# Performance work log

Measured on AMD Instinct MI355X. Metric: run time of the kernel, lower is better.

The kernel has to match this reference:

```python
import jax, jax.numpy as jnp
import numpy as np

N = 100000
E = 1600000
IN_F = 128
OUT_F = 32
HEADS = 6
NEG_SLOPE = 0.2


def setup_inputs() -> dict:
    key = jax.random.key(0)
    k1, k2, k3, k4, k5 = jax.random.split(key, 5)
    x = jax.random.normal(k1, (N, IN_F), dtype=jnp.float32)
    edge_index = jax.random.randint(k2, (2, E), 0, N, dtype=jnp.int64)
    # GATConv params (PyG layout): shared linear for src/dst, per-head attention vectors, bias
    glorot = lambda k, shape: jax.random.normal(k, shape, dtype=jnp.float32) * np.sqrt(2.0 / (shape[0] + shape[-1]))
    W = glorot(k3, (IN_F, HEADS * OUT_F))          # lin.weight^T
    att_src = glorot(k4, (HEADS, OUT_F)) * 0.1     # [H, C]
    att_dst = glorot(k5, (HEADS, OUT_F)) * 0.1
    bias = jnp.zeros((OUT_F,), dtype=jnp.float32)  # concat=False -> bias of size out_feature
    return {"x": x, "edge_index": edge_index, "W": W,
            "att_src": att_src, "att_dst": att_dst, "bias": bias}


def reference(x, edge_index, W, att_src, att_dst, bias):
    src, dst = edge_index[0], edge_index[1]
    # Linear projection to per-head features: [N, H, C]
    xp = (x @ W).reshape(N, HEADS, OUT_F)
    # Per-node attention logit halves: [N, H]
    a_s = jnp.einsum("nhc,hc->nh", xp, att_src)
    a_d = jnp.einsum("nhc,hc->nh", xp, att_dst)
    # Per-edge logits with LeakyReLU: [E, H]
    e = jax.nn.leaky_relu(a_s[src] + a_d[dst], negative_slope=NEG_SLOPE)
    # Segment softmax over edges grouped by destination node
    m = jax.ops.segment_max(e, dst, num_segments=N)            # [N, H]
    m = jnp.where(jnp.isfinite(m), m, 0.0)                     # empty segments -> -inf guard
    e = jnp.exp(e - m[dst])
    s = jax.ops.segment_sum(e, dst, num_segments=N)            # [N, H]
    alpha = e / (s[dst] + 1e-16)                               # [E, H]
    # Weighted scatter-add aggregation: [N, H, C]
    msg = xp[src] * alpha[:, :, None]
    out = jax.ops.segment_sum(msg, dst, num_segments=N)
    # concat=False -> mean over heads, add bias, then SELU
    out = out.mean(axis=1) + bias
    return jax.nn.selu(out)
```

## Files before the change

### kernel.cpp

```cpp
#include <hip/hip_runtime.h>


typedef __attribute__((ext_vector_type(8))) short short8;
typedef __attribute__((ext_vector_type(4))) float f32x4;

#define SK 136
#define SLOTS 48

__device__ __forceinline__ unsigned short f2bf(float f)
{
    unsigned int u = __float_as_uint(f);
    u = (u + 0x7fffu + ((u >> 16) & 1u)) >> 16;
    return (unsigned short)u;
}

__global__ __launch_bounds__(256) void k_prep(
    const float* __restrict__ W,
    const float* __restrict__ att_src, const float* __restrict__ att_dst,
    unsigned short* __restrict__ wat, unsigned short* __restrict__ Wb,
    int* __restrict__ deg, int N)
{
    int i = blockIdx.x * 256 + threadIdx.x;
    if (i < N) deg[i] = 0;
    if (i < 128 * 192) Wb[i] = f2bf(W[i]);
    if (i < 128 * 16) {
        int k = i >> 4, c = i & 15;
        float v = 0.f;
        if (c < 12) {
            int h = c < 6 ? c : c - 6;
            const float* av = (c < 6 ? att_src : att_dst) + h * 32;
            const float* wr = W + k * 192 + h * 32;
            #pragma unroll
            for (int j = 0; j < 32; ++j) v = fmaf(wr[j], av[j], v);
        }
        wat[i] = f2bf(v);
    }
}

__global__ __launch_bounds__(256) void k_gd(
    const float* __restrict__ x, const unsigned short* __restrict__ Wb,
    const unsigned short* __restrict__ wat,
    char* __restrict__ xpb, float* __restrict__ sc,
    float* __restrict__ a_s, float* __restrict__ a_d,
    const int* __restrict__ ei, int* __restrict__ deg, int* __restrict__ csr,
    int N, int E, int GB, int DB)
{
    __shared__ __align__(16) unsigned short xt[64 * SK];
    __shared__ unsigned int smax[64 * 6];
    const int t   = threadIdx.x;
    const int bid = (int)blockIdx.x >> 1;

    if (blockIdx.x & 1) {
        if (bid >= DB) return;
        const int G = DB * 256;
        const int gid = bid * 256 + t;
        int s[4], d[4], r[4];
        #pragma unroll
        for (int k = 0; k < 4; ++k) {
            int e = gid + k * G;
            bool ok = e < E;
            int ec = ok ? e : 0;
            s[k] = ei[ec];
            d[k] = ei[E + ec];
            if (!ok) d[k] = -1;
        }
        #pragma unroll
        for (int k = 0; k < 4; ++k)
            r[k] = (d[k] >= 0) ? atomicAdd(&deg[d[k]], 1) : SLOTS;
        #pragma unroll
        for (int k = 0; k < 4; ++k)
            if (r[k] < SLOTS && d[k] >= 0) csr[d[k] * SLOTS + r[k]] = s[k];
        return;
    }

    if (bid >= GB) return;
    const int wave = t >> 6;
    const int lane = t & 63;
    const int ln   = lane & 15;
    const int q    = lane >> 4;
    const int n0   = bid * 64;
    const int cb   = wave * 48;

    {
        const float4* x4 = (const float4*)x;
        #pragma unroll
        for (int it = 0; it < 8; ++it) {
            int i   = t + it * 256;
            int row = i >> 5;
            int c4  = i & 31;
            int gr  = n0 + row;
            if (gr > N - 1) gr = N - 1;
            float4 f = x4[(size_t)gr * 32 + c4];
            unsigned int u0 = (unsigned int)f2bf(f.x) | ((unsigned int)f2bf(f.y) << 16);
            unsigned int u1 = (unsigned int)f2bf(f.z) | ((unsigned int)f2bf(f.w) << 16);
            *(uint2*)(xt + row * SK + c4 * 4) = make_uint2(u0, u1);
        }
        if (t < 128) { smax[t] = 0u; smax[t + 128] = 0u; smax[t + 256] = 0u; }
    }

    short8 bw[3][4];
    #pragma unroll
    for (int nt = 0; nt < 3; ++nt)
        #pragma unroll
        for (int kbi = 0; kbi < 4; ++kbi) {
            short8 v;
            #pragma unroll
            for (int j = 0; j < 8; ++j)
                v[j] = (short)Wb[(kbi * 32 + q * 8 + j) * 192 + cb + nt * 16 + ln];
            bw[nt][kbi] = v;
        }
    short8 bwa[4];
    #pragma unroll
    for (int kbi = 0; kbi < 4; ++kbi) {
        short8 v;
        #pragma unroll
        for (int j = 0; j < 8; ++j)
            v[j] = (short)wat[(kbi * 32 + q * 8 + j) * 16 + ln];
        bwa[kbi] = v;
    }

    __syncthreads();

    f32x4 acc[4][3];
    #pragma unroll
    for (int mt = 0; mt < 4; ++mt)
        #pragma unroll
        for (int nt = 0; nt < 3; ++nt) acc[mt][nt] = (f32x4)0.f;

    #pragma unroll
    for (int kbi = 0; kbi < 4; ++kbi) {
        #pragma unroll
        for (int mt = 0; mt < 4; ++mt) {
            short8 av = *(const short8*)(xt + (mt * 16 + ln) * SK + kbi * 32 + q * 8);
            #pragma unroll
            for (int nt = 0; nt < 3; ++nt)
                acc[mt][nt] = __builtin_amdgcn_mfma_f32_16x16x32_bf16(
                    av, bw[nt][kbi], acc[mt][nt], 0, 0, 0);
        }
    }

    f32x4 acca = (f32x4)0.f;
    #pragma unroll
    for (int kbi = 0; kbi < 4; ++kbi) {
        short8 av = *(const short8*)(xt + (wave * 16 + ln) * SK + kbi * 32 + q * 8);
        acca = __builtin_amdgcn_mfma_f32_16x16x32_bf16(av, bwa[kbi], acca, 0, 0, 0);
    }

    #pragma unroll
    for (int mt = 0; mt < 4; ++mt) {
        #pragma unroll
        for (int r = 0; r < 4; ++r) {
            int row = mt * 16 + q * 4 + r;
            #pragma unroll
            for (int nt = 0; nt < 3; ++nt) {
                float m = fabsf(acc[mt][nt][r]);
                #pragma unroll
                for (int d = 1; d <= 8; d <<= 1)
                    m = fmaxf(m, __shfl_xor(m, d));
                if (ln == 0) {
                    int head = (cb + nt * 16) >> 5;
                    atomicMax(&smax[row * 6 + head], __float_as_uint(m));
                }
            }
        }
    }
    #pragma unroll
    for (int r = 0; r < 4; ++r) {
        int grow = n0 + wave * 16 + q * 4 + r;
        if (grow < N) {
            if (ln < 6)       a_s[(size_t)grow * 6 + ln]     = acca[r];
            else if (ln < 12) a_d[(size_t)grow * 6 + ln - 6] = acca[r];
        }
    }
    __syncthreads();

    for (int i2 = t; i2 < 384; i2 += 256) {
        int row = i2 / 6, h = i2 - row * 6;
        float m = __uint_as_float(smax[i2]);
        int grow = n0 + row;
        if (grow < N) sc[(size_t)grow * 6 + h] = m * (1.f / 127.f);
        smax[i2] = __float_as_uint(m > 0.f ? 127.f / m : 0.f);
    }
    __syncthreads();

    #pragma unroll
    for (int mt = 0; mt < 4; ++mt) {
        #pragma unroll
        for (int r = 0; r < 4; ++r) {
            int row  = mt * 16 + q * 4 + r;
            int grow = n0 + row;
            if (grow < N) {
                #pragma unroll
                for (int nt = 0; nt < 3; ++nt) {
                    int head = (cb + nt * 16) >> 5;
                    float inv = __uint_as_float(smax[row * 6 + head]);
                    int qv = (int)rintf(acc[mt][nt][r] * inv);
                    xpb[(size_t)grow * 192 + cb + nt * 16 + ln] = (char)qv;
                }
            }
        }
    }
}

__global__ __launch_bounds__(256) void k_agg(
    const char* __restrict__ xpb, const float* __restrict__ sc,
    const float* __restrict__ a_s, const float* __restrict__ a_d,
    const int* __restrict__ csr, const int* __restrict__ degv,
    const float* __restrict__ bias, float* __restrict__ out, int N)
{
    const int wid = threadIdx.x >> 6;
    const int l   = threadIdx.x & 63;
    const int n = blockIdx.x * 4 + wid;
    if (n >= N) return;

    int deg = degv[n];
    deg = deg < SLOTS ? deg : SLOTS;
    const int nb  = n * SLOTS;
    const int hr  = l >> 3;
    const int h   = hr < 6 ? hr : 5;
    const int lc  = l < 48 ? l : 47;
    const unsigned lcb = (unsigned)lc * 4u;
    const unsigned h4  = (unsigned)h * 4u;
    const char* __restrict__ xpB = (const char*)xpb;
    const char* __restrict__ asB = (const char*)a_s;
    const char* __restrict__ scB = (const char*)sc;

    const float zd = a_d[(size_t)n * 6 + h];

    float ax = 0.f, ay = 0.f, az = 0.f, aw = 0.f, se = 0.f;

    int my3 = (l < deg) ? csr[nb + l] * 3 : 0;
    int i = 0;
    for (; i + 8 <= deg; i += 8) {
        unsigned s3[8]; float as[8]; float ss[8]; unsigned int xv[8];
        #pragma unroll
        for (int k = 0; k < 8; ++k) {
            s3[k] = (unsigned)__shfl(my3, i + k);
            as[k] = *(const float*)(asB + s3[k] * 8u + h4);
            ss[k] = *(const float*)(scB + s3[k] * 8u + h4);
        }
        #pragma unroll
        for (int k = 0; k < 8; ++k)
            xv[k] = *(const unsigned int*)(xpB + s3[k] * 64u + lcb);
        #pragma unroll
        for (int k = 0; k < 8; ++k) {
            float z = as[k] + zd;
            z = fmaxf(z, 0.2f * z);
            float ev = __expf(z);
            float evs = ev * ss[k];
            unsigned v = xv[k];
            float f0 = (float)((int)(v << 24) >> 24);
            float f1 = (float)((int)(v << 16) >> 24);
            float f2 = (float)((int)(v <<  8) >> 24);
            float f3 = (float)((int)v >> 24);
            ax = fmaf(evs, f0, ax);
            ay = fmaf(evs, f1, ay);
            az = fmaf(evs, f2, az);
            aw = fmaf(evs, f3, aw);
            se += ev;
        }
    }
    for (; i < deg; ++i) {
        unsigned s3 = (unsigned)__shfl(my3, i);
        float z  = *(const float*)(asB + s3 * 8u + h4) + zd;
        z = fmaxf(z, 0.2f * z);
        float ev = __expf(z);
        float evs = ev * *(const float*)(scB + s3 * 8u + h4);
        unsigned v = *(const unsigned int*)(xpB + s3 * 64u + lcb);
        float f0 = (float)((int)(v << 24) >> 24);
        float f1 = (float)((int)(v << 16) >> 24);
        float f2 = (float)((int)(v <<  8) >> 24);
        float f3 = (float)((int)v >> 24);
        ax = fmaf(evs, f0, ax);
        ay = fmaf(evs, f1, ay);
        az = fmaf(evs, f2, az);
        aw = fmaf(evs, f3, aw);
        se += ev;
    }

    const float inv = 1.f / (se + 1e-16f);
    float v0 = (l < 48) ? ax * inv : 0.f;
    float v1 = (l < 48) ? ay * inv : 0.f;
    float v2 = (l < 48) ? az * inv : 0.f;
    float v3 = (l < 48) ? aw * inv : 0.f;

    #pragma unroll
    for (int d = 8; d <= 32; d <<= 1) {
        v0 += __shfl_down(v0, d);
        v1 += __shfl_down(v1, d);
        v2 += __shfl_down(v2, d);
        v3 += __shfl_down(v3, d);
    }

    if (l < 8) {
        float4 b4 = ((const float4*)bias)[l];
        const float scs = 1.0507009873554805f, al = 1.6732632423543772f;
        float m[4] = {v0 * (1.f / 6.f) + b4.x, v1 * (1.f / 6.f) + b4.y,
                      v2 * (1.f / 6.f) + b4.z, v3 * (1.f / 6.f) + b4.w};
        #pragma unroll
        for (int k = 0; k < 4; ++k)
            m[k] = m[k] > 0.f ? scs * m[k] : scs * al * (__expf(m[k]) - 1.f);
        ((float4*)out)[(size_t)n * 8 + l] = make_float4(m[0], m[1], m[2], m[3]);
    }
}

extern "C" void kernel_launch(void* const* d_in, const int* in_sizes, int n_in,
                              void* d_out, int out_size, void* d_ws, size_t ws_size,
                              hipStream_t stream)
{
    const float* x       = (const float*)d_in[0];
    const int*   ei      = (const int*)d_in[1];
    const float* W       = (const float*)d_in[2];
    const float* att_src = (const float*)d_in[3];
    const float* att_dst = (const float*)d_in[4];
    const float* bias    = (const float*)d_in[5];
    float* out = (float*)d_out;

    const int N = in_sizes[0] / 128;
    const int E = in_sizes[1] / 2;
    const int GB = (N + 63) / 64;
    const int DB = (E + 4 * 256 - 1) / (4 * 256);
    const int MB = (GB > DB ? GB : DB) * 2;

    char* ws = (char*)d_ws;
    size_t o = 0;
    auto take = [&](size_t bytes) { size_t r = o; o = (o + bytes + 255) & ~(size_t)255; return r; };
    char*  xpb     = (char*) (ws + take((size_t)N * 192));
    float* sc      = (float*)(ws + take((size_t)N * 6 * 4));
    float* a_s     = (float*)(ws + take((size_t)N * 6 * 4));
    float* a_d     = (float*)(ws + take((size_t)N * 6 * 4));
    int*   deg     = (int*)  (ws + take((size_t)N * 4));
    int*   csr     = (int*)  (ws + take((size_t)N * SLOTS * 4));
    unsigned short* wat = (unsigned short*)(ws + take((size_t)128 * 16 * 2));
    unsigned short* Wb  = (unsigned short*)(ws + take((size_t)128 * 192 * 2));
    (void)ws_size; (void)n_in; (void)out_size;

    int pg = (N + 255) / 256;
    k_prep<<<pg, 256, 0, stream>>>(W, att_src, att_dst, wat, Wb, deg, N);
    k_gd<<<MB, 256, 0, stream>>>(x, Wb, wat, xpb, sc, a_s, a_d,
                                 ei, deg, csr, N, E, GB, DB);
    k_agg<<<(N + 3) / 4, 256, 0, stream>>>(xpb, sc, a_s, a_d, csr, deg, bias, out, N);
}
```

Baseline: 277.2 us.

## Interleave a_s and scale into float2 and store xp as offset-uint8

Packs the per-node attention half a_s and the int8 quantization scale into one float2 array, so the aggregation gather does one 8-byte load per neighbor instead of two scattered 4-byte loads. Quantized features are stored as unsigned bytes with a +128 offset, so unpacking is plain shift-and-mask with unsigned conversion. The offset is removed at the end by subtracting 128 times the running sum of scaled weights. This adds one accumulator per lane and some rounding error from the offset correction.

```diff
diff --git a/kernel.cpp b/kernel.cpp
--- a/kernel.cpp
+++ b/kernel.cpp
@@ -40,8 +40,8 @@
 __global__ __launch_bounds__(256) void k_gd(
     const float* __restrict__ x, const unsigned short* __restrict__ Wb,
     const unsigned short* __restrict__ wat,
-    char* __restrict__ xpb, float* __restrict__ sc,
-    float* __restrict__ a_s, float* __restrict__ a_d,
+    unsigned char* __restrict__ xpb, float2* __restrict__ asc,
+    float* __restrict__ a_d,
     const int* __restrict__ ei, int* __restrict__ deg, int* __restrict__ csr,
     int N, int E, int GB, int DB)
 {
@@ -168,7 +168,7 @@
     for (int r = 0; r < 4; ++r) {
         int grow = n0 + wave * 16 + q * 4 + r;
         if (grow < N) {
-            if (ln < 6)       a_s[(size_t)grow * 6 + ln]     = acca[r];
+            if (ln < 6)       asc[(size_t)grow * 6 + ln].x   = acca[r];
             else if (ln < 12) a_d[(size_t)grow * 6 + ln - 6] = acca[r];
         }
     }
@@ -178,7 +178,7 @@
         int row = i2 / 6, h = i2 - row * 6;
         float m = __uint_as_float(smax[i2]);
         int grow = n0 + row;
-        if (grow < N) sc[(size_t)grow * 6 + h] = m * (1.f / 127.f);
+        if (grow < N) asc[(size_t)grow * 6 + h].y = m * (1.f / 127.f);
         smax[i2] = __float_as_uint(m > 0.f ? 127.f / m : 0.f);
     }
     __syncthreads();
@@ -194,8 +194,8 @@
                 for (int nt = 0; nt < 3; ++nt) {
                     int head = (cb + nt * 16) >> 5;
                     float inv = __uint_as_float(smax[row * 6 + head]);
-                    int qv = (int)rintf(acc[mt][nt][r] * inv);
-                    xpb[(size_t)grow * 192 + cb + nt * 16 + ln] = (char)qv;
+                    int qv = (int)rintf(acc[mt][nt][r] * inv) + 128;
+                    xpb[(size_t)grow * 192 + cb + nt * 16 + ln] = (unsigned char)qv;
                 }
             }
         }
@@ -203,8 +203,8 @@
 }
 
 __global__ __launch_bounds__(256) void k_agg(
-    const char* __restrict__ xpb, const float* __restrict__ sc,
-    const float* __restrict__ a_s, const float* __restrict__ a_d,
+    const unsigned char* __restrict__ xpb, const float2* __restrict__ asc,
+    const float* __restrict__ a_d,
     const int* __restrict__ csr, const int* __restrict__ degv,
     const float* __restrict__ bias, float* __restrict__ out, int N)
 {
@@ -220,69 +220,71 @@
     const int h   = hr < 6 ? hr : 5;
     const int lc  = l < 48 ? l : 47;
     const unsigned lcb = (unsigned)lc * 4u;
-    const unsigned h4  = (unsigned)h * 4u;
-    const char* __restrict__ xpB = (const char*)xpb;
-    const char* __restrict__ asB = (const char*)a_s;
-    const char* __restrict__ scB = (const char*)sc;
+    const unsigned h8  = (unsigned)h * 8u;
+    const char* __restrict__ xpB  = (const char*)xpb;
+    const char* __restrict__ ascB = (const char*)asc;
 
     const float zd = a_d[(size_t)n * 6 + h];
 
-    float ax = 0.f, ay = 0.f, az = 0.f, aw = 0.f, se = 0.f;
+    float ax = 0.f, ay = 0.f, az = 0.f, aw = 0.f, se = 0.f, sevs = 0.f;
 
     int my3 = (l < deg) ? csr[nb + l] * 3 : 0;
     int i = 0;
     for (; i + 8 <= deg; i += 8) {
-        unsigned s3[8]; float as[8]; float ss[8]; unsigned int xv[8];
+        unsigned s3[8]; float2 av[8]; unsigned int xv[8];
         #pragma unroll
         for (int k = 0; k < 8; ++k) {
             s3[k] = (unsigned)__shfl(my3, i + k);
-            as[k] = *(const float*)(asB + s3[k] * 8u + h4);
-            ss[k] = *(const float*)(scB + s3[k] * 8u + h4);
+            av[k] = *(const float2*)(ascB + s3[k] * 16u + h8);
         }
         #pragma unroll
         for (int k = 0; k < 8; ++k)
             xv[k] = *(const unsigned int*)(xpB + s3[k] * 64u + lcb);
         #pragma unroll
         for (int k = 0; k < 8; ++k) {
-            float z = as[k] + zd;
+            float z = av[k].x + zd;
             z = fmaxf(z, 0.2f * z);
             float ev = __expf(z);
-            float evs = ev * ss[k];
+            float evs = ev * av[k].y;
             unsigned v = xv[k];
-            float f0 = (float)((int)(v << 24) >> 24);
-            float f1 = (float)((int)(v << 16) >> 24);
-            float f2 = (float)((int)(v <<  8) >> 24);
-            float f3 = (float)((int)v >> 24);
+            float f0 = (float)(v & 0xffu);
+            float f1 = (float)((v >> 8) & 0xffu);
+            float f2 = (float)((v >> 16) & 0xffu);
+            float f3 = (float)(v >> 24);
             ax = fmaf(evs, f0, ax);
             ay = fmaf(evs, f1, ay);
             az = fmaf(evs, f2, az);
             aw = fmaf(evs, f3, aw);
             se += ev;
+            sevs += evs;
         }
     }
     for (; i < deg; ++i) {
         unsigned s3 = (unsigned)__shfl(my3, i);
-        float z  = *(const float*)(asB + s3 * 8u + h4) + zd;
+        float2 av = *(const float2*)(ascB + s3 * 16u + h8);
+        float z = av.x + zd;
         z = fmaxf(z, 0.2f * z);
         float ev = __expf(z);
-        float evs = ev * *(const float*)(scB + s3 * 8u + h4);
+        float evs = ev * av.y;
         unsigned v = *(const unsigned int*)(xpB + s3 * 64u + lcb);
-        float f0 = (float)((int)(v << 24) >> 24);
-        float f1 = (float)((int)(v << 16) >> 24);
-        float f2 = (float)((int)(v <<  8) >> 24);
-        float f3 = (float)((int)v >> 24);
+        float f0 = (float)(v & 0xffu);
+        float f1 = (float)((v >> 8) & 0xffu);
+        float f2 = (float)((v >> 16) & 0xffu);
+        float f3 = (float)(v >> 24);
         ax = fmaf(evs, f0, ax);
         ay = fmaf(evs, f1, ay);
         az = fmaf(evs, f2, az);
         aw = fmaf(evs, f3, aw);
         se += ev;
-    }
-
+        sevs += evs;
+    }
+
+    const float cor = 128.f * sevs;
     const float inv = 1.f / (se + 1e-16f);
-    float v0 = (l < 48) ? ax * inv : 0.f;
-    float v1 = (l < 48) ? ay * inv : 0.f;
-    float v2 = (l < 48) ? az * inv : 0.f;
-    float v3 = (l < 48) ? aw * inv : 0.f;
+    float v0 = (l < 48) ? (ax - cor) * inv : 0.f;
+    float v1 = (l < 48) ? (ay - cor) * inv : 0.f;
+    float v2 = (l < 48) ? (az - cor) * inv : 0.f;
+    float v3 = (l < 48) ? (aw - cor) * inv : 0.f;
 
     #pragma unroll
     for (int d = 8; d <= 32; d <<= 1) {
@@ -325,19 +327,18 @@
     char* ws = (char*)d_ws;
     size_t o = 0;
     auto take = [&](size_t bytes) { size_t r = o; o = (o + bytes + 255) & ~(size_t)255; return r; };
-    char*  xpb     = (char*) (ws + take((size_t)N * 192));
-    float* sc      = (float*)(ws + take((size_t)N * 6 * 4));
-    float* a_s     = (float*)(ws + take((size_t)N * 6 * 4));
-    float* a_d     = (float*)(ws + take((size_t)N * 6 * 4));
-    int*   deg     = (int*)  (ws + take((size_t)N * 4));
-    int*   csr     = (int*)  (ws + take((size_t)N * SLOTS * 4));
+    unsigned char* xpb = (unsigned char*)(ws + take((size_t)N * 192));
+    float2* asc    = (float2*)(ws + take((size_t)N * 6 * 8));
+    float*  a_d    = (float*) (ws + take((size_t)N * 6 * 4));
+    int*    deg    = (int*)   (ws + take((size_t)N * 4));
+    int*    csr    = (int*)   (ws + take((size_t)N * SLOTS * 4));
     unsigned short* wat = (unsigned short*)(ws + take((size_t)128 * 16 * 2));
     unsigned short* Wb  = (unsigned short*)(ws + take((size_t)128 * 192 * 2));
     (void)ws_size; (void)n_in; (void)out_size;
 
     int pg = (N + 255) / 256;
     k_prep<<<pg, 256, 0, stream>>>(W, att_src, att_dst, wat, Wb, deg, N);
-    k_gd<<<MB, 256, 0, stream>>>(x, Wb, wat, xpb, sc, a_s, a_d,
+    k_gd<<<MB, 256, 0, stream>>>(x, Wb, wat, xpb, asc, a_d,
                                  ei, deg, csr, N, E, GB, DB);
-    k_agg<<<(N + 3) / 4, 256, 0, stream>>>(xpb, sc, a_s, a_d, csr, deg, bias, out, N);
-}
+    k_agg<<<(N + 3) / 4, 256, 0, stream>>>(xpb, asc, a_d, csr, deg, bias, out, N);
+}
```

After: 270.2 us. -2.5%, faster.
